# Optimization experiments

Hardware: AMD Instinct MI355X
Metric: run time of the kernel (lower is better)

Reference implementation:

```python
import jax, jax.numpy as jnp
import numpy as np

D = 128      # entity_and_theorem_embedding_size
M = 8192     # nodes per tree level
L = 5        # internal (non-leaf) levels
V = 4096     # number of input entities (leaf vocab)
K = 8        # number of binary numerical functions
KL = 4       # number of binary logic functions
G = 4096     # number of ground-truth logic statements


def setup_inputs() -> dict:
    key = jax.random.key(0)
    ks = jax.random.split(key, 16)
    s = 0.05
    return {
        "leaf_ids": jax.random.randint(ks[0], (M,), 0, V, dtype=jnp.int32),
        "left_idx": jax.random.randint(ks[1], (L, M), 0, M, dtype=jnp.int32),
        "right_idx": jax.random.randint(ks[2], (L, M), 0, M, dtype=jnp.int32),
        "nf_fid": jax.random.randint(ks[3], (L, M), 0, K, dtype=jnp.int32),
        "gt_left": jax.random.randint(ks[4], (G,), 0, M, dtype=jnp.int32),
        "gt_right": jax.random.randint(ks[5], (G,), 0, M, dtype=jnp.int32),
        "lf_fid": jax.random.randint(ks[6], (G,), 0, KL, dtype=jnp.int32),
        "emb": jax.random.normal(ks[7], (V, D), jnp.float32),
        "W1": jax.random.normal(ks[8], (K, 2 * D, 4 * D), jnp.float32) * s,
        "b1": jnp.zeros((K, 4 * D), jnp.float32),
        "W2": jax.random.normal(ks[9], (K, 4 * D, 2 * D), jnp.float32) * s,
        "b2": jnp.zeros((K, 2 * D), jnp.float32),
        "W3": jax.random.normal(ks[10], (K, 2 * D, D), jnp.float32) * s,
        "b3": jnp.zeros((K, D), jnp.float32),
        "Wl1": jax.random.normal(ks[11], (KL, 2 * D, 4 * D), jnp.float32) * s,
        "bl1": jnp.zeros((KL, 4 * D), jnp.float32),
        "Wl2": jax.random.normal(ks[12], (KL, 4 * D, D), jnp.float32) * s,
        "bl2": jnp.zeros((KL, D), jnp.float32),
    }


def _select(y, fid):
    # y: [N, K, F], fid: [N] -> [N, F]  (per-node dynamic MLP dispatch)
    return jnp.take_along_axis(y, fid[:, None, None], axis=1)[:, 0, :]


def reference(leaf_ids, left_idx, right_idx, nf_fid, gt_left, gt_right, lf_fid,
              emb, W1, b1, W2, b2, W3, b3, Wl1, bl1, Wl2, bl2):
    # Leaf entities: embedding lookup (input_entity_embedding)
    h0 = emb[leaf_ids]  # [M, D]

    # Internal entity nodes: recursive nf_two2one MLPs, level-synchronous
    def level(h, xs):
        li, ri, fid = xs
        x = jnp.concatenate([h[li], h[ri]], axis=-1)          # [M, 2D] concat of operands
        a1 = jax.nn.relu(jnp.einsum('nd,kdf->nkf', x, W1) + b1)   # [M, K, 4D]
        a2 = jax.nn.relu(jnp.einsum('nkd,kdf->nkf', a1, W2) + b2) # [M, K, 2D]
        a3 = jnp.einsum('nkd,kdf->nkf', a2, W3) + b3              # [M, K, D]
        return _select(a3, fid), None
    hL, _ = jax.lax.scan(level, h0, (left_idx, right_idx, nf_fid))

    # Logic statements: lf_two2one MLP on pairs of entity encodings
    xg = jnp.concatenate([hL[gt_left], hL[gt_right]], axis=-1)    # [G, 2D]
    g1 = jax.nn.relu(jnp.einsum('nd,kdf->nkf', xg, Wl1) + bl1)    # [G, KL, 4D]
    g2 = jnp.einsum('nkd,kdf->nkf', g1, Wl2) + bl2                # [G, KL, D]
    return _select(g2, lf_fid)                                    # [G, D]
```

## Files before the change

### kernel.cpp

```cpp
#include <hip/hip_runtime.h>

constexpr int D  = 128;
constexpr int M  = 8192;
constexpr int L  = 5;
constexpr int K  = 8;
constexpr int KL = 4;
constexpr int G  = 4096;

constexpr int TB   = 64;
constexpr int PADL = M + K * TB;
constexpr int PADG = G + KL * TB;

typedef short bf16x8 __attribute__((ext_vector_type(8)));
typedef float f32x4  __attribute__((ext_vector_type(4)));

__device__ __forceinline__ unsigned short f2bf(float x) {
  union { float f; unsigned int u; } c; c.f = x;
  unsigned int u = c.u + 0x7FFF + ((c.u >> 16) & 1);
  return (unsigned short)(u >> 16);
}
__device__ __forceinline__ float bf2f(unsigned short h) {
  union { unsigned int u; float f; } c; c.u = ((unsigned int)h) << 16;
  return c.f;
}

__global__ void leaf_gather_kernel(const int* __restrict__ leaf_ids,
                                   const float* __restrict__ emb,
                                   float* __restrict__ h0) {
  int idx = blockIdx.x * 256 + threadIdx.x;
  int n = idx >> 7, d = idx & 127;
  h0[idx] = emb[(size_t)leaf_ids[n] * D + d];
}

__global__ void bucket64_kernel(const int* __restrict__ nf_fid,
                                const int* __restrict__ lf_fid,
                                int* __restrict__ orders) {
  int b = blockIdx.x;
  const int* fid; int N, Kf, cap; int* out;
  if (b < L) { fid = nf_fid + b * M; N = M; Kf = K;  cap = PADL; out = orders + b * PADL; }
  else       { fid = lf_fid;         N = G; Kf = KL; cap = PADG; out = orders + L * PADL; }
  __shared__ int cnt[8];
  __shared__ int cur[8];
  int tid = threadIdx.x;
  if (tid < Kf) cnt[tid] = 0;
  __syncthreads();
  for (int i = tid; i < N; i += 256) atomicAdd(&cnt[fid[i]], 1);
  __syncthreads();
  if (tid == 0) {
    int off = 0;
    for (int k = 0; k < Kf; ++k) { cur[k] = off; off += ((cnt[k] + TB - 1) / TB) * TB; }
  }
  __syncthreads();
  for (int i = tid; i < cap; i += 256) out[i] = -1;
  __syncthreads();
  for (int i = tid; i < N; i += 256) {
    int kk = fid[i];
    int pos = atomicAdd(&cur[kk], 1);
    out[pos] = i;
  }
}

__global__ void prep_kernel(const float* __restrict__ W1, const float* __restrict__ W2,
                            const float* __restrict__ W3, const float* __restrict__ Wl1,
                            const float* __restrict__ Wl2,
                            short* __restrict__ B1T, short* __restrict__ B2T,
                            short* __restrict__ B3T, short* __restrict__ BL1T,
                            short* __restrict__ BL2T) {
  int b = blockIdx.x;
  const float* W; short* BT; int KD, F;
  if      (b < 4096) { W = W1;  BT = B1T;  KD = 256; F = 512; }
  else if (b < 6144) { W = W2;  BT = B2T;  KD = 512; F = 256; b -= 4096; }
  else if (b < 7168) { W = W3;  BT = B3T;  KD = 256; F = 128; b -= 6144; }
  else if (b < 9216) { W = Wl1; BT = BL1T; KD = 256; F = 512; b -= 7168; }
  else               { W = Wl2; BT = BL2T; KD = 512; F = 128; b -= 9216; }
  int k = b / F, f = b % F;
  for (int d = threadIdx.x; d < KD; d += 256) {
    float w = W[((size_t)k * KD + d) * F + f];
    unsigned short hi = f2bf(w);
    unsigned short lo = f2bf(w - bf2f(hi));
    BT[((size_t)k * F + f) * (2 * KD) + d]      = (short)hi;
    BT[((size_t)k * F + f) * (2 * KD) + KD + d] = (short)lo;
  }
}

template<int KH, int NN, int EPI, int FUSED, int TROWS>
__global__ __launch_bounds__(256) void mfma_gemm(
    const short* __restrict__ A, const float* __restrict__ hsrc,
    const int* __restrict__ gl, const int* __restrict__ gr,
    const short* __restrict__ BT, const float* __restrict__ bias,
    short* __restrict__ Aout, float* __restrict__ outp,
    const int* __restrict__ order, const int* __restrict__ fid) {
  static_assert(FUSED == 0 || TROWS == 64, "fused gather assumes 64-row tiles");
  constexpr int BK  = 64;
  constexpr int NCH = 3 * KH / BK;
  constexpr int LDA = BK + 8;
  constexpr int RF  = TROWS / 32;
  constexpr int TPR = 256 / TROWS;
  __shared__ __align__(16) short As[TROWS * LDA];
  __shared__ __align__(16) short Bs[128 * LDA];
  __shared__ int nodesS[TROWS], liS[TROWS], riS[TROWS];

  const int tid = threadIdx.x;
  const int row0 = blockIdx.x * TROWS;
  const int ct = blockIdx.y;

  if (tid < TROWS) {
    int node = order[row0 + tid];
    nodesS[tid] = node;
    if (FUSED) {
      liS[tid] = node >= 0 ? gl[node] : 0;
      riS[tid] = node >= 0 ? gr[node] : 0;
    }
  }
  __syncthreads();
  if (nodesS[0] < 0) return;
  const int kfn = fid[nodesS[0]];
  const short* __restrict__ Bk = BT + (size_t)kfn * NN * (2 * KH);

  const int lane = tid & 63, wave = tid >> 6;
  const int wr = (wave >> 1) * (TROWS / 2);
  const int wc = wave & 1;
  const int l15 = lane & 15, oct = lane >> 4;

  const int ar = tid / TPR;
  const int ag = (tid % TPR) * (BK / TPR);
  const int bn = tid >> 1;
  const int bg = (tid & 1) * 32;

  f32x4 acc[RF][4];
  #pragma unroll
  for (int i = 0; i < RF; ++i)
    #pragma unroll
    for (int j = 0; j < 4; ++j) acc[i][j] = (f32x4)0.f;

  int4 A00, A01, A10, A11;
  float4 F00, F01, F02, F03, F10, F11, F12, F13;
  int4 B00, B01, B02, B03, B10, B11, B12, B13;

  auto loadB_to = [&](int c, int4& r0, int4& r1, int4& r2, int4& r3) {
    int ko = c * BK, seg = ko / KH, wi = ko % KH;
    int pb = (seg == 2) ? KH + wi : wi;
    const int4* p = (const int4*)(Bk + (size_t)(ct * 128 + bn) * (2 * KH) + pb + bg);
    r0 = p[0]; r1 = p[1]; r2 = p[2]; r3 = p[3];
  };
  auto loadA_to = [&](int c, int4& r0, int4& r1,
                      float4& f0, float4& f1, float4& f2, float4& f3) {
    int ko = c * BK, seg = ko / KH, wi = ko % KH;
    if (FUSED) {
      int dl = wi + ag;
      if (nodesS[ar] >= 0) {
        const float* src = (dl < 128) ? (hsrc + (size_t)liS[ar] * 128 + dl)
                                      : (hsrc + (size_t)riS[ar] * 128 + (dl - 128));
        const float4* p = (const float4*)src;
        f0 = p[0]; f1 = p[1]; f2 = p[2]; f3 = p[3];
      } else {
        f0 = f1 = f2 = f3 = make_float4(0.f, 0.f, 0.f, 0.f);
      }
    } else {
      int pa = (seg == 1) ? KH + wi : wi;
      const int4* p = (const int4*)(A + (size_t)(row0 + ar) * (2 * KH) + pa + ag);
      r0 = p[0];
      if (TPR == 4) r1 = p[1];
    }
  };
  auto storeLDS_from = [&](int c, int4& r0, int4& r1,
                           float4& f0, float4& f1, float4& f2, float4& f3,
                           int4& b0, int4& b1, int4& b2, int4& b3) {
    if (FUSED) {
      int seg = (c * BK) / KH;
      float v[16];
      ((float4*)v)[0] = f0; ((float4*)v)[1] = f1;
      ((float4*)v)[2] = f2; ((float4*)v)[3] = f3;
      union { unsigned short u[16]; int4 q[2]; } o;
      if (seg != 1) {
        #pragma unroll
        for (int i = 0; i < 16; ++i) o.u[i] = f2bf(v[i]);
      } else {
        #pragma unroll
        for (int i = 0; i < 16; ++i) {
          unsigned short hh = f2bf(v[i]);
          o.u[i] = f2bf(v[i] - bf2f(hh));
        }
      }
      int4* d4 = (int4*)&As[ar * LDA + ag];
      d4[0] = o.q[0]; d4[1] = o.q[1];
    } else {
      int4* d4 = (int4*)&As[ar * LDA + ag];
      d4[0] = r0;
      if (TPR == 4) d4[1] = r1;
    }
    int4* db = (int4*)&Bs[bn * LDA + bg];
    db[0] = b0; db[1] = b1; db[2] = b2; db[3] = b3;
  };
  auto compute = [&]() {
    #pragma unroll
    for (int s = 0; s < 2; ++s) {
      const int ko = s * 32 + oct * 8;
      bf16x8 afr[RF];
      #pragma unroll
      for (int rf = 0; rf < RF; ++rf)
        afr[rf] = *(const bf16x8*)&As[(wr + rf * 16 + l15) * LDA + ko];
      #pragma unroll
      for (int cf = 0; cf < 4; ++cf) {
        bf16x8 b = *(const bf16x8*)&Bs[(wc * 64 + cf * 16 + l15) * LDA + ko];
        #pragma unroll
        for (int rf = 0; rf < RF; ++rf)
          acc[rf][cf] = __builtin_amdgcn_mfma_f32_16x16x32_bf16(afr[rf], b, acc[rf][cf], 0, 0, 0);
      }
    }
  };

  loadA_to(0, A00, A01, F00, F01, F02, F03);
  loadB_to(0, B00, B01, B02, B03);
  loadA_to(1, A10, A11, F10, F11, F12, F13);
  loadB_to(1, B10, B11, B12, B13);
  for (int c = 0; c < NCH; c += 2) {
    __syncthreads();
    storeLDS_from(c, A00, A01, F00, F01, F02, F03, B00, B01, B02, B03);
    __syncthreads();
    if (c + 2 < NCH) {
      loadA_to(c + 2, A00, A01, F00, F01, F02, F03);
      loadB_to(c + 2, B00, B01, B02, B03);
    }
    compute();
    __syncthreads();
    storeLDS_from(c + 1, A10, A11, F10, F11, F12, F13, B10, B11, B12, B13);
    __syncthreads();
    if (c + 3 < NCH) {
      loadA_to(c + 3, A10, A11, F10, F11, F12, F13);
      loadB_to(c + 3, B10, B11, B12, B13);
    }
    compute();
  }

  if (EPI == 0) {
    short* Ls = (short*)Bs;
    #pragma unroll
    for (int part = 0; part < 2; ++part) {
      __syncthreads();
      #pragma unroll
      for (int rf = 0; rf < RF; ++rf)
        #pragma unroll
        for (int cf = 0; cf < 4; ++cf) {
          int colL = wc * 64 + cf * 16 + l15;
          float bv = bias[kfn * NN + ct * 128 + colL];
          #pragma unroll
          for (int j = 0; j < 4; ++j) {
            int row = wr + rf * 16 + oct * 4 + j;
            float v = fmaxf(acc[rf][cf][j] + bv, 0.f);
            unsigned short hh = f2bf(v);
            unsigned short val = (part == 0) ? hh : f2bf(v - bf2f(hh));
            Ls[row * 128 + colL] = (short)val;
          }
        }
      __syncthreads();
      constexpr int SPT = TROWS / 2;
      constexpr int TPW = 128 / SPT;
      int row = tid / TPW, sg = (tid % TPW) * SPT;
      const int4* src = (const int4*)&Ls[row * 128 + sg];
      int4* dst = (int4*)&Aout[(size_t)(row0 + row) * (2 * NN) + part * NN + ct * 128 + sg];
      #pragma unroll
      for (int q = 0; q < SPT / 8; ++q) dst[q] = src[q];
    }
  } else {
    float* Lf = (float*)Bs;
    #pragma unroll
    for (int h = 0; h < 2; ++h) {
      __syncthreads();
      if (wc == h) {
        #pragma unroll
        for (int rf = 0; rf < RF; ++rf)
          #pragma unroll
          for (int cf = 0; cf < 4; ++cf) {
            int colL = cf * 16 + l15;
            float bv = bias[kfn * 128 + h * 64 + colL];
            #pragma unroll
            for (int j = 0; j < 4; ++j) {
              int row = wr + rf * 16 + oct * 4 + j;
              Lf[row * 64 + colL] = acc[rf][cf][j] + bv;
            }
          }
      }
      __syncthreads();
      constexpr int FPT = TROWS / 4;
      constexpr int TPW = 64 / FPT;
      int row = tid / TPW, off = (tid % TPW) * FPT;
      int node = nodesS[row];
      if (node >= 0) {
        const float4* src = (const float4*)&Lf[row * 64 + off];
        float4* dst = (float4*)&outp[(size_t)node * 128 + h * 64 + off];
        #pragma unroll
        for (int q = 0; q < FPT / 4; ++q) dst[q] = src[q];
      }
    }
  }
}

extern "C" void kernel_launch(void* const* d_in, const int* in_sizes, int n_in,
                              void* d_out, int out_size, void* d_ws, size_t ws_size,
                              hipStream_t stream) {
  const int*   leaf_ids  = (const int*)d_in[0];
  const int*   left_idx  = (const int*)d_in[1];
  const int*   right_idx = (const int*)d_in[2];
  const int*   nf_fid    = (const int*)d_in[3];
  const int*   gt_left   = (const int*)d_in[4];
  const int*   gt_right  = (const int*)d_in[5];
  const int*   lf_fid    = (const int*)d_in[6];
  const float* emb       = (const float*)d_in[7];
  const float* W1 = (const float*)d_in[8];
  const float* b1 = (const float*)d_in[9];
  const float* W2 = (const float*)d_in[10];
  const float* b2 = (const float*)d_in[11];
  const float* W3 = (const float*)d_in[12];
  const float* b3 = (const float*)d_in[13];
  const float* Wl1 = (const float*)d_in[14];
  const float* bl1 = (const float*)d_in[15];
  const float* Wl2 = (const float*)d_in[16];
  const float* bl2 = (const float*)d_in[17];
  float* out = (float*)d_out;

  const size_t SZ_H    = (size_t)M * D * 4;
  const size_t SZ_A1   = (size_t)PADL * 1024 * 2;
  const size_t SZ_A2   = (size_t)PADL * 512 * 2;
  const size_t SZ_B1T  = (size_t)8 * 512 * 512 * 2;
  const size_t SZ_B2T  = (size_t)8 * 256 * 1024 * 2;
  const size_t SZ_B3T  = (size_t)8 * 128 * 512 * 2;
  const size_t SZ_BL1T = (size_t)4 * 512 * 512 * 2;
  const size_t SZ_BL2T = (size_t)4 * 128 * 1024 * 2;

  char* p = (char*)d_ws;
  float* hA   = (float*)p;  p += SZ_H;
  float* hB   = (float*)p;  p += SZ_H;
  short* a1s  = (short*)p;  p += SZ_A1;
  short* a2s  = (short*)p;  p += SZ_A2;
  short* B1T  = (short*)p;  p += SZ_B1T;
  short* B2T  = (short*)p;  p += SZ_B2T;
  short* B3T  = (short*)p;  p += SZ_B3T;
  short* BL1T = (short*)p;  p += SZ_BL1T;
  short* BL2T = (short*)p;  p += SZ_BL2T;
  int*   orders = (int*)p;

  leaf_gather_kernel<<<(M * D) / 256, 256, 0, stream>>>(leaf_ids, emb, hA);
  bucket64_kernel<<<L + 1, 256, 0, stream>>>(nf_fid, lf_fid, orders);
  prep_kernel<<<9728, 256, 0, stream>>>(W1, W2, W3, Wl1, Wl2,
                                        B1T, B2T, B3T, BL1T, BL2T);

  float* hin = hA;
  float* hout = hB;
  for (int l = 0; l < L; ++l) {
    const int* ord = orders + l * PADL;
    const int* fidl = nf_fid + l * M;
    mfma_gemm<256, 512, 0, 1, 64><<<dim3(PADL / 64, 4), 256, 0, stream>>>(
        nullptr, hin, left_idx + l * M, right_idx + l * M,
        B1T, b1, a1s, nullptr, ord, fidl);
    mfma_gemm<512, 256, 0, 0, 64><<<dim3(PADL / 64, 2), 256, 0, stream>>>(
        a1s, nullptr, nullptr, nullptr,
        B2T, b2, a2s, nullptr, ord, fidl);
    mfma_gemm<256, 128, 1, 0, 32><<<dim3(PADL / 32, 1), 256, 0, stream>>>(
        a2s, nullptr, nullptr, nullptr,
        B3T, b3, nullptr, hout, ord, fidl);
    float* t = hin; hin = hout; hout = t;
  }
  const int* ordG = orders + L * PADL;
  mfma_gemm<256, 512, 0, 1, 64><<<dim3(PADG / 64, 4), 256, 0, stream>>>(
      nullptr, hin, gt_left, gt_right,
      BL1T, bl1, a1s, nullptr, ordG, lf_fid);
  mfma_gemm<512, 128, 1, 0, 32><<<dim3(PADG / 32, 1), 256, 0, stream>>>(
      a1s, nullptr, nullptr, nullptr,
      BL2T, bl2, nullptr, out, ordG, lf_fid);
}
```

Baseline: 515.4 us.

## Shrink GEMM tiles to 32 rows and split-K the output GEMMs into partial buffers

Every GEMM now uses 32-row tiles, so more blocks are launched. The final-layer GEMMs (EPI==1) are split over the K dimension into two z-slices, and each slice writes its own partial output buffer. The next level's fused gather sums the two partials on load. A separate add kernel combines the partials for the final output. This targets low occupancy on the narrow output GEMMs, at the cost of extra partial buffers, duplicated gather reads and one extra kernel launch.

Result: slower. 1.232 ms (+139.0%).

```diff
diff --git a/kernel.cpp b/kernel.cpp
--- a/kernel.cpp
+++ b/kernel.cpp
@@ -30,6 +30,13 @@
   int idx = blockIdx.x * 256 + threadIdx.x;
   int n = idx >> 7, d = idx & 127;
   h0[idx] = emb[(size_t)leaf_ids[n] * D + d];
+}
+
+__global__ void add_out_kernel(const float* __restrict__ o0,
+                               const float* __restrict__ o1,
+                               float* __restrict__ out) {
+  int idx = blockIdx.x * 256 + threadIdx.x;
+  out[idx] = o0[idx] + o1[idx];
 }
 
 __global__ void bucket64_kernel(const int* __restrict__ nf_fid,
@@ -83,28 +90,27 @@
   }
 }
 
-template<int KH, int NN, int EPI, int FUSED, int TROWS>
+template<int KH, int NN, int EPI, int FUSED, int SUMIN>
 __global__ __launch_bounds__(256) void mfma_gemm(
-    const short* __restrict__ A, const float* __restrict__ hsrc,
+    const short* __restrict__ A,
+    const float* __restrict__ h0, const float* __restrict__ h1,
     const int* __restrict__ gl, const int* __restrict__ gr,
     const short* __restrict__ BT, const float* __restrict__ bias,
-    short* __restrict__ Aout, float* __restrict__ outp,
+    short* __restrict__ Aout, float* __restrict__ outp, size_t partStride,
     const int* __restrict__ order, const int* __restrict__ fid) {
-  static_assert(FUSED == 0 || TROWS == 64, "fused gather assumes 64-row tiles");
   constexpr int BK  = 64;
   constexpr int NCH = 3 * KH / BK;
   constexpr int LDA = BK + 8;
-  constexpr int RF  = TROWS / 32;
-  constexpr int TPR = 256 / TROWS;
-  __shared__ __align__(16) short As[TROWS * LDA];
+  __shared__ __align__(16) short As[32 * LDA];
   __shared__ __align__(16) short Bs[128 * LDA];
-  __shared__ int nodesS[TROWS], liS[TROWS], riS[TROWS];
+  __shared__ int nodesS[32], liS[32], riS[32];
 
   const int tid = threadIdx.x;
-  const int row0 = blockIdx.x * TROWS;
+  const int row0 = blockIdx.x * 32;
   const int ct = blockIdx.y;
-
-  if (tid < TROWS) {
+  const int z  = blockIdx.z;
+
+  if (tid < 32) {
     int node = order[row0 + tid];
     nodesS[tid] = node;
     if (FUSED) {
@@ -118,118 +124,115 @@
   const short* __restrict__ Bk = BT + (size_t)kfn * NN * (2 * KH);
 
   const int lane = tid & 63, wave = tid >> 6;
-  const int wr = (wave >> 1) * (TROWS / 2);
-  const int wc = wave & 1;
   const int l15 = lane & 15, oct = lane >> 4;
-
-  const int ar = tid / TPR;
-  const int ag = (tid % TPR) * (BK / TPR);
-  const int bn = tid >> 1;
+  const int wcol = wave * 32;
+
+  const int ar = tid >> 3;
+  const int ag = (tid & 7) * 8;
+  const int bcol = tid >> 1;
   const int bg = (tid & 1) * 32;
 
-  f32x4 acc[RF][4];
+  const int c0 = (EPI == 1) ? z * (NCH / 2) : 0;
+  const int CN = (EPI == 1) ? (NCH / 2) : NCH;
+
+  f32x4 acc[2][2];
   #pragma unroll
-  for (int i = 0; i < RF; ++i)
+  for (int i = 0; i < 2; ++i)
     #pragma unroll
-    for (int j = 0; j < 4; ++j) acc[i][j] = (f32x4)0.f;
-
-  int4 A00, A01, A10, A11;
-  float4 F00, F01, F02, F03, F10, F11, F12, F13;
-  int4 B00, B01, B02, B03, B10, B11, B12, B13;
-
-  auto loadB_to = [&](int c, int4& r0, int4& r1, int4& r2, int4& r3) {
+    for (int j = 0; j < 2; ++j) acc[i][j] = (f32x4)0.f;
+
+  int4 A0r, A1r;
+  float4 F0a, F0b, F0c, F0d, F1a, F1b, F1c, F1d;
+  int4 B0r[4], B1r[4];
+
+  auto loadB_to = [&](int c, int4* r) {
     int ko = c * BK, seg = ko / KH, wi = ko % KH;
     int pb = (seg == 2) ? KH + wi : wi;
-    const int4* p = (const int4*)(Bk + (size_t)(ct * 128 + bn) * (2 * KH) + pb + bg);
-    r0 = p[0]; r1 = p[1]; r2 = p[2]; r3 = p[3];
+    const int4* p = (const int4*)(Bk + (size_t)(ct * 128 + bcol) * (2 * KH) + pb + bg);
+    r[0] = p[0]; r[1] = p[1]; r[2] = p[2]; r[3] = p[3];
   };
-  auto loadA_to = [&](int c, int4& r0, int4& r1,
-                      float4& f0, float4& f1, float4& f2, float4& f3) {
+  auto loadA_to = [&](int c, int4& r0,
+                      float4& fa, float4& fb, float4& fc, float4& fd) {
     int ko = c * BK, seg = ko / KH, wi = ko % KH;
     if (FUSED) {
       int dl = wi + ag;
       if (nodesS[ar] >= 0) {
-        const float* src = (dl < 128) ? (hsrc + (size_t)liS[ar] * 128 + dl)
-                                      : (hsrc + (size_t)riS[ar] * 128 + (dl - 128));
-        const float4* p = (const float4*)src;
-        f0 = p[0]; f1 = p[1]; f2 = p[2]; f3 = p[3];
+        size_t off = (dl < 128) ? ((size_t)liS[ar] * 128 + dl)
+                                : ((size_t)riS[ar] * 128 + (dl - 128));
+        const float4* p0 = (const float4*)(h0 + off);
+        fa = p0[0]; fb = p0[1];
+        if (SUMIN) {
+          const float4* p1 = (const float4*)(h1 + off);
+          fc = p1[0]; fd = p1[1];
+        }
       } else {
-        f0 = f1 = f2 = f3 = make_float4(0.f, 0.f, 0.f, 0.f);
+        fa = fb = fc = fd = make_float4(0.f, 0.f, 0.f, 0.f);
       }
     } else {
       int pa = (seg == 1) ? KH + wi : wi;
-      const int4* p = (const int4*)(A + (size_t)(row0 + ar) * (2 * KH) + pa + ag);
-      r0 = p[0];
-      if (TPR == 4) r1 = p[1];
+      r0 = *(const int4*)(A + (size_t)(row0 + ar) * (2 * KH) + pa + ag);
     }
   };
-  auto storeLDS_from = [&](int c, int4& r0, int4& r1,
-                           float4& f0, float4& f1, float4& f2, float4& f3,
-                           int4& b0, int4& b1, int4& b2, int4& b3) {
+  auto storeLDS_from = [&](int c, int4& r0,
+                           float4& fa, float4& fb, float4& fc, float4& fd,
+                           int4* br) {
     if (FUSED) {
       int seg = (c * BK) / KH;
-      float v[16];
-      ((float4*)v)[0] = f0; ((float4*)v)[1] = f1;
-      ((float4*)v)[2] = f2; ((float4*)v)[3] = f3;
-      union { unsigned short u[16]; int4 q[2]; } o;
+      float v[8];
+      ((float4*)v)[0] = fa; ((float4*)v)[1] = fb;
+      if (SUMIN) {
+        float w[8];
+        ((float4*)w)[0] = fc; ((float4*)w)[1] = fd;
+        #pragma unroll
+        for (int i = 0; i < 8; ++i) v[i] += w[i];
+      }
+      union { unsigned short u[8]; int4 q; } o;
       if (seg != 1) {
         #pragma unroll
-        for (int i = 0; i < 16; ++i) o.u[i] = f2bf(v[i]);
+        for (int i = 0; i < 8; ++i) o.u[i] = f2bf(v[i]);
       } else {
         #pragma unroll
-        for (int i = 0; i < 16; ++i) {
+        for (int i = 0; i < 8; ++i) {
           unsigned short hh = f2bf(v[i]);
           o.u[i] = f2bf(v[i] - bf2f(hh));
         }
       }
-      int4* d4 = (int4*)&As[ar * LDA + ag];
-      d4[0] = o.q[0]; d4[1] = o.q[1];
+      *(int4*)&As[ar * LDA + ag] = o.q;
     } else {
-      int4* d4 = (int4*)&As[ar * LDA + ag];
-      d4[0] = r0;
-      if (TPR == 4) d4[1] = r1;
-    }
-    int4* db = (int4*)&Bs[bn * LDA + bg];
-    db[0] = b0; db[1] = b1; db[2] = b2; db[3] = b3;
+      *(int4*)&As[ar * LDA + ag] = r0;
+    }
+    int4* db = (int4*)&Bs[bcol * LDA + bg];
+    db[0] = br[0]; db[1] = br[1]; db[2] = br[2]; db[3] = br[3];
   };
   auto compute = [&]() {
     #pragma unroll
     for (int s = 0; s < 2; ++s) {
       const int ko = s * 32 + oct * 8;
-      bf16x8 afr[RF];
+      bf16x8 a0 = *(const bf16x8*)&As[(l15) * LDA + ko];
+      bf16x8 a1 = *(const bf16x8*)&As[(16 + l15) * LDA + ko];
       #pragma unroll
-      for (int rf = 0; rf < RF; ++rf)
-        afr[rf] = *(const bf16x8*)&As[(wr + rf * 16 + l15) * LDA + ko];
-      #pragma unroll
-      for (int cf = 0; cf < 4; ++cf) {
-        bf16x8 b = *(const bf16x8*)&Bs[(wc * 64 + cf * 16 + l15) * LDA + ko];
-        #pragma unroll
-        for (int rf = 0; rf < RF; ++rf)
-          acc[rf][cf] = __builtin_amdgcn_mfma_f32_16x16x32_bf16(afr[rf], b, acc[rf][cf], 0, 0, 0);
+      for (int cf = 0; cf < 2; ++cf) {
+        bf16x8 b = *(const bf16x8*)&Bs[(wcol + cf * 16 + l15) * LDA + ko];
+        acc[0][cf] = __builtin_amdgcn_mfma_f32_16x16x32_bf16(a0, b, acc[0][cf], 0, 0, 0);
+        acc[1][cf] = __builtin_amdgcn_mfma_f32_16x16x32_bf16(a1, b, acc[1][cf], 0, 0, 0);
       }
     }
   };
 
-  loadA_to(0, A00, A01, F00, F01, F02, F03);
-  loadB_to(0, B00, B01, B02, B03);
-  loadA_to(1, A10, A11, F10, F11, F12, F13);
-  loadB_to(1, B10, B11, B12, B13);
-  for (int c = 0; c < NCH; c += 2) {
-    __syncthreads();
-    storeLDS_from(c, A00, A01, F00, F01, F02, F03, B00, B01, B02, B03);
-    __syncthreads();
-    if (c + 2 < NCH) {
-      loadA_to(c + 2, A00, A01, F00, F01, F02, F03);
-      loadB_to(c + 2, B00, B01, B02, B03);
-    }
+  loadA_to(c0, A0r, F0a, F0b, F0c, F0d);
+  loadB_to(c0, B0r);
+  loadA_to(c0 + 1, A1r, F1a, F1b, F1c, F1d);
+  loadB_to(c0 + 1, B1r);
+  for (int c = 0; c < CN; c += 2) {
+    __syncthreads();
+    storeLDS_from(c0 + c, A0r, F0a, F0b, F0c, F0d, B0r);
+    __syncthreads();
+    if (c + 2 < CN) { loadA_to(c0 + c + 2, A0r, F0a, F0b, F0c, F0d); loadB_to(c0 + c + 2, B0r); }
     compute();
     __syncthreads();
-    storeLDS_from(c + 1, A10, A11, F10, F11, F12, F13, B10, B11, B12, B13);
-    __syncthreads();
-    if (c + 3 < NCH) {
-      loadA_to(c + 3, A10, A11, F10, F11, F12, F13);
-      loadB_to(c + 3, B10, B11, B12, B13);
-    }
+    storeLDS_from(c0 + c + 1, A1r, F1a, F1b, F1c, F1d, B1r);
+    __syncthreads();
+    if (c + 3 < CN) { loadA_to(c0 + c + 3, A1r, F1a, F1b, F1c, F1d); loadB_to(c0 + c + 3, B1r); }
     compute();
   }
 
@@ -239,14 +242,14 @@
     for (int part = 0; part < 2; ++part) {
       __syncthreads();
       #pragma unroll
-      for (int rf = 0; rf < RF; ++rf)
-        #pragma unroll
-        for (int cf = 0; cf < 4; ++cf) {
-          int colL = wc * 64 + cf * 16 + l15;
+      for (int rf = 0; rf < 2; ++rf)
+        #pragma unroll
+        for (int cf = 0; cf < 2; ++cf) {
+          int colL = wcol + cf * 16 + l15;
           float bv = bias[kfn * NN + ct * 128 + colL];
           #pragma unroll
           for (int j = 0; j < 4; ++j) {
-            int row = wr + rf * 16 + oct * 4 + j;
+            int row = rf * 16 + oct * 4 + j;
             float v = fmaxf(acc[rf][cf][j] + bv, 0.f);
             unsigned short hh = f2bf(v);
             unsigned short val = (part == 0) ? hh : f2bf(v - bf2f(hh));
@@ -254,44 +257,34 @@
           }
         }
       __syncthreads();
-      constexpr int SPT = TROWS / 2;
-      constexpr int TPW = 128 / SPT;
-      int row = tid / TPW, sg = (tid % TPW) * SPT;
+      int row = tid >> 3, sg = (tid & 7) * 16;
       const int4* src = (const int4*)&Ls[row * 128 + sg];
       int4* dst = (int4*)&Aout[(size_t)(row0 + row) * (2 * NN) + part * NN + ct * 128 + sg];
-      #pragma unroll
-      for (int q = 0; q < SPT / 8; ++q) dst[q] = src[q];
+      dst[0] = src[0]; dst[1] = src[1];
     }
   } else {
     float* Lf = (float*)Bs;
+    __syncthreads();
     #pragma unroll
-    for (int h = 0; h < 2; ++h) {
-      __syncthreads();
-      if (wc == h) {
-        #pragma unroll
-        for (int rf = 0; rf < RF; ++rf)
-          #pragma unroll
-          for (int cf = 0; cf < 4; ++cf) {
-            int colL = cf * 16 + l15;
-            float bv = bias[kfn * 128 + h * 64 + colL];
-            #pragma unroll
-            for (int j = 0; j < 4; ++j) {
-              int row = wr + rf * 16 + oct * 4 + j;
-              Lf[row * 64 + colL] = acc[rf][cf][j] + bv;
-            }
-          }
-      }
-      __syncthreads();
-      constexpr int FPT = TROWS / 4;
-      constexpr int TPW = 64 / FPT;
-      int row = tid / TPW, off = (tid % TPW) * FPT;
-      int node = nodesS[row];
-      if (node >= 0) {
-        const float4* src = (const float4*)&Lf[row * 64 + off];
-        float4* dst = (float4*)&outp[(size_t)node * 128 + h * 64 + off];
-        #pragma unroll
-        for (int q = 0; q < FPT / 4; ++q) dst[q] = src[q];
-      }
+    for (int rf = 0; rf < 2; ++rf)
+      #pragma unroll
+      for (int cf = 0; cf < 2; ++cf) {
+        int colL = wcol + cf * 16 + l15;
+        float bv = (z == 0) ? bias[kfn * 128 + colL] : 0.f;
+        #pragma unroll
+        for (int j = 0; j < 4; ++j) {
+          int row = rf * 16 + oct * 4 + j;
+          Lf[row * 128 + colL] = acc[rf][cf][j] + bv;
+        }
+      }
+    __syncthreads();
+    float* outz = outp + (size_t)z * partStride;
+    int row = tid >> 3, fo = (tid & 7) * 16;
+    int node = nodesS[row];
+    if (node >= 0) {
+      const float4* src = (const float4*)&Lf[row * 128 + fo];
+      float4* dst = (float4*)&outz[(size_t)node * 128 + fo];
+      dst[0] = src[0]; dst[1] = src[1]; dst[2] = src[2]; dst[3] = src[3];
     }
   }
 }
@@ -320,6 +313,7 @@
   float* out = (float*)d_out;
 
   const size_t SZ_H    = (size_t)M * D * 4;
+  const size_t SZ_O    = (size_t)G * D * 4;
   const size_t SZ_A1   = (size_t)PADL * 1024 * 2;
   const size_t SZ_A2   = (size_t)PADL * 512 * 2;
   const size_t SZ_B1T  = (size_t)8 * 512 * 512 * 2;
@@ -329,15 +323,20 @@
   const size_t SZ_BL2T = (size_t)4 * 128 * 1024 * 2;
 
   char* p = (char*)d_ws;
-  float* hA   = (float*)p;  p += SZ_H;
-  float* hB   = (float*)p;  p += SZ_H;
-  short* a1s  = (short*)p;  p += SZ_A1;
-  short* a2s  = (short*)p;  p += SZ_A2;
-  short* B1T  = (short*)p;  p += SZ_B1T;
-  short* B2T  = (short*)p;  p += SZ_B2T;
-  short* B3T  = (short*)p;  p += SZ_B3T;
-  short* BL1T = (short*)p;  p += SZ_BL1T;
-  short* BL2T = (short*)p;  p += SZ_BL2T;
+  float* hA  = (float*)p;  p += SZ_H;
+  float* p0  = (float*)p;  p += SZ_H;
+  float* p1  = (float*)p;  p += SZ_H;
+  float* q0  = (float*)p;  p += SZ_H;
+  float* q1  = (float*)p;  p += SZ_H;
+  float* o0  = (float*)p;  p += SZ_O;
+  float* o1  = (float*)p;  p += SZ_O;
+  short* a1s = (short*)p;  p += SZ_A1;
+  short* a2s = (short*)p;  p += SZ_A2;
+  short* B1T  = (short*)p; p += SZ_B1T;
+  short* B2T  = (short*)p; p += SZ_B2T;
+  short* B3T  = (short*)p; p += SZ_B3T;
+  short* BL1T = (short*)p; p += SZ_BL1T;
+  short* BL2T = (short*)p; p += SZ_BL2T;
   int*   orders = (int*)p;
 
   leaf_gather_kernel<<<(M * D) / 256, 256, 0, stream>>>(leaf_ids, emb, hA);
@@ -345,27 +344,36 @@
   prep_kernel<<<9728, 256, 0, stream>>>(W1, W2, W3, Wl1, Wl2,
                                         B1T, B2T, B3T, BL1T, BL2T);
 
-  float* hin = hA;
-  float* hout = hB;
+  const size_t HSTRIDE = (size_t)M * D;
+  float* in0 = hA; float* in1 = nullptr;
+  float* ou0 = q0; float* ou1 = q1;
   for (int l = 0; l < L; ++l) {
     const int* ord = orders + l * PADL;
     const int* fidl = nf_fid + l * M;
-    mfma_gemm<256, 512, 0, 1, 64><<<dim3(PADL / 64, 4), 256, 0, stream>>>(
-        nullptr, hin, left_idx + l * M, right_idx + l * M,
-        B1T, b1, a1s, nullptr, ord, fidl);
-    mfma_gemm<512, 256, 0, 0, 64><<<dim3(PADL / 64, 2), 256, 0, stream>>>(
-        a1s, nullptr, nullptr, nullptr,
-        B2T, b2, a2s, nullptr, ord, fidl);
-    mfma_gemm<256, 128, 1, 0, 32><<<dim3(PADL / 32, 1), 256, 0, stream>>>(
-        a2s, nullptr, nullptr, nullptr,
-        B3T, b3, nullptr, hout, ord, fidl);
-    float* t = hin; hin = hout; hout = t;
+    if (l == 0) {
+      mfma_gemm<256, 512, 0, 1, 0><<<dim3(PADL / 32, 4, 1), 256, 0, stream>>>(
+          nullptr, in0, nullptr, left_idx + l * M, right_idx + l * M,
+          B1T, b1, a1s, nullptr, 0, ord, fidl);
+    } else {
+      mfma_gemm<256, 512, 0, 1, 1><<<dim3(PADL / 32, 4, 1), 256, 0, stream>>>(
+          nullptr, in0, in1, left_idx + l * M, right_idx + l * M,
+          B1T, b1, a1s, nullptr, 0, ord, fidl);
+    }
+    mfma_gemm<512, 256, 0, 0, 0><<<dim3(PADL / 32, 2, 1), 256, 0, stream>>>(
+        a1s, nullptr, nullptr, nullptr, nullptr,
+        B2T, b2, a2s, nullptr, 0, ord, fidl);
+    mfma_gemm<256, 128, 1, 0, 0><<<dim3(PADL / 32, 1, 2), 256, 0, stream>>>(
+        a2s, nullptr, nullptr, nullptr, nullptr,
+        B3T, b3, nullptr, ou0, HSTRIDE, ord, fidl);
+    in0 = ou0; in1 = ou1;
+    if (ou0 == q0) { ou0 = p0; ou1 = p1; } else { ou0 = q0; ou1 = q1; }
   }
   const int* ordG = orders + L * PADL;
-  mfma_gemm<256, 512, 0, 1, 64><<<dim3(PADG / 64, 4), 256, 0, stream>>>(
-      nullptr, hin, gt_left, gt_right,
-      BL1T, bl1, a1s, nullptr, ordG, lf_fid);
-  mfma_gemm<512, 128, 1, 0, 32><<<dim3(PADG / 32, 1), 256, 0, stream>>>(
-      a1s, nullptr, nullptr, nullptr,
-      BL2T, bl2, nullptr, out, ordG, lf_fid);
-}
+  mfma_gemm<256, 512, 0, 1, 1><<<dim3(PADG / 32, 4, 1), 256, 0, stream>>>(
+      nullptr, in0, in1, gt_left, gt_right,
+      BL1T, bl1, a1s, nullptr, 0, ordG, lf_fid);
+  mfma_gemm<512, 128, 1, 0, 0><<<dim3(PADG / 32, 1, 2), 256, 0, stream>>>(
+      a1s, nullptr, nullptr, nullptr, nullptr,
+      BL2T, bl2, nullptr, o0, (size_t)G * D, ordG, lf_fid);
+  add_out_kernel<<<(G * D) / 256, 256, 0, stream>>>(o0, o1, out);
+}
```
